# Performance work log

Hardware: AMD Instinct MI355X
Metric: run time of the kernel (lower is better)

The kernel has to match this reference:

```python
import jax, jax.numpy as jnp
import numpy as np

N = 8192   # max_nodes
E = 8192   # max_edges
D = 128    # node / edge feature dim


def setup_inputs() -> dict:
    key = jax.random.key(0)
    ks = jax.random.split(key, 6)
    nodes = jax.random.normal(ks[0], (N, D), jnp.float32)
    edges = jax.random.normal(ks[1], (E, D), jnp.float32)
    send = jax.random.randint(ks[2], (E,), 0, N, jnp.int32)
    rec = jax.random.randint(ks[3], (E,), 0, N, jnp.int32)
    # prefix activity masks (standard for this growing-graph module)
    anodes = (jnp.arange(N) < 6144).astype(jnp.float32)
    aedges = (jnp.arange(E) < 2048).astype(jnp.float32)
    Wq = jax.random.normal(ks[4], (D, D), jnp.float32) / np.sqrt(D)
    bq = jnp.zeros((D,), jnp.float32)
    Wp = jax.random.normal(ks[5], (D, 1), jnp.float32) * 0.1
    bp = jnp.full((1,), -5.0, jnp.float32)
    return dict(nodes=nodes, edges=edges, rec=rec, send=send, anodes=anodes,
                aedges=aedges, Wq=Wq, bq=bq, Wp=Wp, bp=bp)


def reference(nodes, edges, rec, send, anodes, aedges, Wq, bq, Wp, bp):
    # fixed PRNG key (the module takes a key argument; we pin it for determinism)
    key = jax.random.key(42)
    key_prob, key_edges, key_samp = jax.random.split(key, 3)

    nids = jnp.arange(N)
    e_active = aedges.sum().astype(jnp.int32)

    # 1. per-node edge-generation probability: prob_fn(h_i) = sigmoid(h_i @ Wp + bp)
    probs = jax.nn.sigmoid(nodes @ Wp + bp)[:, 0]            # [N]
    # 2. sample generating nodes (only active ones)
    gens = (jax.random.uniform(key_prob, (N,)) < probs * anodes).astype(jnp.float32)

    allowed = E - e_active - 1
    n_gens = jnp.clip(gens.astype(jnp.int32).sum(), 0, allowed)

    # grow active-edge mask by n_gens via repeated (mask @ incr_matrix) clip steps
    # incr_matrix(E) = I + superdiagonal, so one step extends a prefix mask by 1
    mat_e = jnp.eye(E, dtype=jnp.float32) + jnp.eye(E, k=1, dtype=jnp.float32)
    naedges = jax.lax.fori_loop(
        0, n_gens, lambda i, x: jnp.clip(x @ mat_e, 0.0, 1.0), aedges
    ).at[-1].set(0.0)
    mask_new = naedges * (1.0 - aedges)                       # [E] newly-created slots

    # 6. new edges get random embeddings in the newly-activated slots
    new_edges = edges + jax.random.normal(key_edges, edges.shape) * mask_new[:, None]

    # cumsum-derived scatter targets: k-th generating node -> edge slot e_active+k
    gi = gens.astype(jnp.int32)
    trgets = jnp.where(gens > 0, (jnp.cumsum(gens) * gens - gens).astype(jnp.int32), -1) \
             + e_active * gi                                   # [N], -1 dropped by segment_sum

    nsend = jax.ops.segment_sum(nids, trgets, num_segments=E)
    nsend = (send * (1.0 - mask_new) + nsend).astype(jnp.int32)

    # 3-5. queries, all-pairs scores, masked categorical target sampling
    queries = nodes @ Wq + bq                                  # [N, D]
    scores = jnp.clip(queries @ nodes.T, -1e4, 1e4)            # [N, N]
    scores = scores - (1.0 - anodes[None, :]) * 1e10
    select = jnp.where(gens > 0,
                       jax.random.categorical(key_samp, scores, axis=-1),
                       0).astype(jnp.int32)                    # [N]

    nrec = jax.ops.segment_sum(select, trgets, num_segments=E)
    nrec = (rec * (1.0 - mask_new) + nrec).astype(jnp.int32)

    return new_edges, nsend, nrec, naedges
```

## Files before the change

kernel.cpp:

```cpp
#include <hip/hip_runtime.h>
#include <stdint.h>
#include <math.h>

#define NN 8192
#define EE 8192
#define DD 128

__host__ __device__ inline void tf2x32(uint32_t k0, uint32_t k1, uint32_t c0, uint32_t c1,
                                       uint32_t& o0, uint32_t& o1) {
  uint32_t ks[3] = {k0, k1, 0x1BD11BDAu ^ k0 ^ k1};
  uint32_t x0 = c0 + k0, x1 = c1 + k1;
  const uint32_t rot0[4] = {13u, 15u, 26u, 6u};
  const uint32_t rot1[4] = {17u, 29u, 16u, 24u};
#pragma unroll
  for (int i = 0; i < 5; ++i) {
#pragma unroll
    for (int r = 0; r < 4; ++r) {
      uint32_t d = (i & 1) ? rot1[r] : rot0[r];
      x0 += x1;
      x1 = (x1 << d) | (x1 >> (32u - d));
      x1 ^= x0;
    }
    x0 += ks[(i + 1) % 3];
    x1 += ks[(i + 2) % 3] + (uint32_t)(i + 1);
  }
  o0 = x0; o1 = x1;
}

__device__ inline uint32_t rbits32(uint32_t k0, uint32_t k1, uint32_t idx) {
  uint32_t o0, o1;
  tf2x32(k0, k1, 0u, idx, o0, o1);
  return o0 ^ o1;
}

__device__ inline float u01(uint32_t b) {
  return __uint_as_float((b >> 9) | 0x3f800000u) - 1.0f;
}

__device__ inline float erfinv_f32(float x) {
  float w = -log1pf(-x * x);
  float p;
  if (w < 5.0f) {
    w -= 2.5f;
    p = 2.81022636e-08f;
    p = fmaf(p, w, 3.43273939e-07f);
    p = fmaf(p, w, -3.5233877e-06f);
    p = fmaf(p, w, -4.39150654e-06f);
    p = fmaf(p, w, 0.00021858087f);
    p = fmaf(p, w, -0.00125372503f);
    p = fmaf(p, w, -0.00417768164f);
    p = fmaf(p, w, 0.246640727f);
    p = fmaf(p, w, 1.50140941f);
  } else {
    w = sqrtf(w) - 3.0f;
    p = -0.000200214257f;
    p = fmaf(p, w, 0.000100950558f);
    p = fmaf(p, w, 0.00134934322f);
    p = fmaf(p, w, -0.00367342844f);
    p = fmaf(p, w, 0.00573950773f);
    p = fmaf(p, w, -0.0076224613f);
    p = fmaf(p, w, 0.00943887047f);
    p = fmaf(p, w, 1.00167406f);
    p = fmaf(p, w, 2.83297682f);
  }
  return p * x;
}

__global__ __launch_bounds__(256)
void k_gens(const float* __restrict__ nodes, const float* __restrict__ Wp,
            const float* __restrict__ bp, const float* __restrict__ anodes,
            int* __restrict__ gens, uint32_t kp0, uint32_t kp1) {
  int t = blockIdx.x * 256 + threadIdx.x;
  int i = t >> 2, qd = t & 3;
  if (i >= NN) return;
  const float4* row = (const float4*)(nodes + (size_t)i * DD);
  const float4* w = (const float4*)Wp;
  float acc = 0.f;
#pragma unroll
  for (int c = 0; c < 8; ++c) {
    int k4 = qd + 4 * c;
    float4 a = row[k4], b = w[k4];
    acc = fmaf(a.x, b.x, acc); acc = fmaf(a.y, b.y, acc);
    acc = fmaf(a.z, b.z, acc); acc = fmaf(a.w, b.w, acc);
  }
  acc += __shfl_xor(acc, 1, 4);
  acc += __shfl_xor(acc, 2, 4);
  if (qd == 0) {
    float prob = 1.0f / (1.0f + expf(-(acc + bp[0])));
    uint32_t b = rbits32(kp0, kp1, (uint32_t)i);
    gens[i] = (u01(b) < prob * anodes[i]) ? 1 : 0;
  }
}

__global__ __launch_bounds__(256)
void k_scan(const float* __restrict__ aedges, const int* __restrict__ gens,
            int* __restrict__ gen_list, float* __restrict__ mask_new,
            float* __restrict__ naedges_out, int* __restrict__ scal,
            unsigned long long* __restrict__ partial) {
  __shared__ int P[EE];
  __shared__ int aux[8];
  int tid = threadIdx.x;
  int base = tid * 32;
  int lane = tid & 63, wid = tid >> 6;

  int av[32]; int aloc = 0;
  {
    const float4* a4 = (const float4*)(aedges + base);
#pragma unroll
    for (int k4 = 0; k4 < 8; ++k4) {
      float4 x = a4[k4];
      av[4 * k4 + 0] = (x.x > 0.f); av[4 * k4 + 1] = (x.y > 0.f);
      av[4 * k4 + 2] = (x.z > 0.f); av[4 * k4 + 3] = (x.w > 0.f);
    }
#pragma unroll
    for (int k = 0; k < 32; ++k) aloc += av[k];
  }
  int incl = aloc;
#pragma unroll
  for (int d = 1; d < 64; d <<= 1) {
    int o = __shfl_up(incl, d, 64);
    if (lane >= d) incl += o;
  }
  if (lane == 63) aux[wid] = incl;

  int g[32]; int gloc = 0;
  {
    const int4* g4 = (const int4*)(gens + base);
#pragma unroll
    for (int k4 = 0; k4 < 8; ++k4) {
      int4 x = g4[k4];
      g[4 * k4 + 0] = x.x; g[4 * k4 + 1] = x.y;
      g[4 * k4 + 2] = x.z; g[4 * k4 + 3] = x.w;
    }
#pragma unroll
    for (int k = 0; k < 32; ++k) gloc += g[k];
  }
  int incg = gloc;
#pragma unroll
  for (int d = 1; d < 64; d <<= 1) {
    int o = __shfl_up(incg, d, 64);
    if (lane >= d) incg += o;
  }
  if (lane == 63) aux[4 + wid] = incg;
  __syncthreads();

  int e_active = aux[0] + aux[1] + aux[2] + aux[3];
  int total = aux[4] + aux[5] + aux[6] + aux[7];
  int wpreA = 0, wpreG = 0;
  for (int ww = 0; ww < wid; ++ww) { wpreA += aux[ww]; wpreG += aux[4 + ww]; }

  {
    int run = wpreA + incl - aloc;
#pragma unroll
    for (int k = 0; k < 32; ++k) { run += av[k]; P[base + k] = run; }
  }
  {
    int rank = wpreG + incg - gloc;
#pragma unroll
    for (int k = 0; k < 32; ++k) {
      if (g[k]) {
        if (e_active + rank < EE) gen_list[rank] = base + k;
        rank++;
      }
    }
  }
  if (tid == 0) { scal[0] = e_active; scal[1] = total; }

  for (int idx = tid; idx < total * 32; idx += 256) partial[idx] = 0ull;

  int allowed = EE - e_active - 1;
  int n_gens = total;
  if (n_gens > allowed) n_gens = allowed;
  if (n_gens < 0) n_gens = 0;

  __syncthreads();
#pragma unroll
  for (int k = 0; k < 32; ++k) {
    int j = base + k;
    int lo = j - n_gens - 1;
    int wsum = P[j] - (lo >= 0 ? P[lo] : 0);
    float dil = (wsum > 0) ? 1.f : 0.f;
    if (j == EE - 1) dil = 0.f;
    naedges_out[j] = dil;
    mask_new[j] = dil * (1.0f - (float)av[k]);
  }
}

__global__ __launch_bounds__(128)
void k_queries(const float* __restrict__ nodes, const float* __restrict__ Wq,
               const float* __restrict__ bq, const int* __restrict__ gen_list,
               const int* __restrict__ scal, float* __restrict__ queries) {
  __shared__ float ni[DD];
  int tid = threadIdx.x;
  int total = scal[1];
  for (int r = blockIdx.x; r < total; r += gridDim.x) {
    int i = gen_list[r];
    ni[tid] = nodes[(size_t)i * DD + tid];
    __syncthreads();
    float acc = bq[tid];
    for (int k = 0; k < DD; ++k) acc = fmaf(ni[k], Wq[k * DD + tid], acc);
    queries[(size_t)r * DD + tid] = acc;
    __syncthreads();
  }
}

__global__ __launch_bounds__(256)
void k_score(const float* __restrict__ nodes, const float* __restrict__ anodes,
             const float* __restrict__ queries, const int* __restrict__ gen_list,
             const int* __restrict__ scal, unsigned long long* __restrict__ partial,
             uint32_t ks0, uint32_t ks1) {
  __shared__ float4 nd[32 * 32];
  __shared__ float q[8][DD];
  __shared__ float an[32];
  __shared__ int gi[8];
  int tid = threadIdx.x;
  int j0 = blockIdx.x * 32;
  int total = scal[1];
  int rt0 = blockIdx.y * 8;
  if (rt0 >= total) return;

  {
    int jj = tid >> 3, sub = tid & 7;
    const float4* src = (const float4*)(nodes + (size_t)(j0 + jj) * DD);
#pragma unroll
    for (int c = 0; c < 4; ++c) {
      int k4 = sub + 8 * c;
      nd[jj * 32 + ((k4 + jj) & 31)] = src[k4];
    }
    if (tid < 32) an[tid] = anodes[j0 + tid];
  }

  int rr = tid >> 5, jl = tid & 31;
  for (int rb = rt0; rb < total; rb += 8 * gridDim.y) {
    __syncthreads();
    {
      int lr = rb + (tid >> 5);
      int k4 = tid & 31;
      if (lr < total) {
        ((float4*)q[tid >> 5])[k4] = ((const float4*)(queries + (size_t)lr * DD))[k4];
        if (k4 == 0) gi[tid >> 5] = gen_list[lr];
      }
    }
    __syncthreads();

    int r = rb + rr;
    if (r < total) {
      const float4* qv = (const float4*)q[rr];
      float acc = 0.f;
#pragma unroll
      for (int k4 = 0; k4 < 32; ++k4) {
        float4 n = nd[jl * 32 + ((k4 + jl) & 31)];
        float4 qq = qv[k4];
        acc = fmaf(n.x, qq.x, acc); acc = fmaf(n.y, qq.y, acc);
        acc = fmaf(n.z, qq.z, acc); acc = fmaf(n.w, qq.w, acc);
      }
      int j = j0 + jl;
      float sc = fminf(fmaxf(acc, -1e4f), 1e4f);
      sc -= (1.0f - an[jl]) * 1e10f;
      uint32_t bidx = (uint32_t)gi[rr] * NN + (uint32_t)j;
      uint32_t b = rbits32(ks0, ks1, bidx);
      float u = fmaxf(1.17549435e-38f, u01(b));
      float gmb = -logf(-logf(u));
      float v = sc + gmb;
      int jbest = j;
#pragma unroll
      for (int m = 16; m; m >>= 1) {
        float ov = __shfl_xor(v, m, 32);
        int oj = __shfl_xor(jbest, m, 32);
        if (ov > v || (ov == v && oj < jbest)) { v = ov; jbest = oj; }
      }
      if (jl == 0) {
        uint32_t fb = __float_as_uint(v);
        fb = (fb & 0x80000000u) ? ~fb : (fb | 0x80000000u);
        unsigned long long key =
            ((unsigned long long)fb << 32) | (uint32_t)(NN - 1 - jbest);
        atomicMax(&partial[(size_t)r * 32 + (blockIdx.x >> 3)], key);
      }
    }
  }
}

__global__ __launch_bounds__(256)
void k_post(const float* __restrict__ edges, const float* __restrict__ mask_new,
            const int* __restrict__ send, const int* __restrict__ rec,
            const int* __restrict__ gen_list,
            const unsigned long long* __restrict__ partial,
            const int* __restrict__ scal,
            float* __restrict__ out_edges, float* __restrict__ out_nsend,
            float* __restrict__ out_nrec, uint32_t ke0, uint32_t ke1) {
  int t = blockIdx.x * 256 + threadIdx.x;
  int idx = t * 4;
  int e = idx >> 7;
  float m = mask_new[e];
  float4 v = ((const float4*)edges)[t];
  if (m > 0.f) {
    float* pv = &v.x;
#pragma unroll
    for (int k = 0; k < 4; ++k) {
      uint32_t b = rbits32(ke0, ke1, (uint32_t)(idx + k));
      float u = u01(b);
      float x = fmaf(u, 2.0f, -0.99999994f);
      x = fmaxf(-0.99999994f, x);
      float nrm = 1.41421354f * erfinv_f32(x);
      pv[k] += nrm * m;
    }
  }
  ((float4*)out_edges)[t] = v;

  if (t < EE) {
    int e_active = scal[0], total = scal[1];
    float mm = mask_new[t];
    float sf = (float)send[t] * (1.0f - mm);
    float rf = (float)rec[t] * (1.0f - mm);
    int r = t - e_active;
    if (r >= 0 && r < total) {
      unsigned long long best = 0ull;
      const unsigned long long* pp = partial + (size_t)r * 32;
#pragma unroll
      for (int p = 0; p < 32; ++p) { unsigned long long x = pp[p]; if (x > best) best = x; }
      int i = gen_list[r];
      int jsel = (NN - 1) - (int)(best & 0xFFFFFFFFull);
      sf += (float)i;
      rf += (float)jsel;
    }
    out_nsend[t] = (float)(int)sf;
    out_nrec[t] = (float)(int)rf;
  }
}

extern "C" void kernel_launch(void* const* d_in, const int* in_sizes, int n_in,
                              void* d_out, int out_size, void* d_ws, size_t ws_size,
                              hipStream_t stream) {
  const float* nodes  = (const float*)d_in[0];
  const float* edges  = (const float*)d_in[1];
  const int*   rec    = (const int*)d_in[2];
  const int*   send   = (const int*)d_in[3];
  const float* anodes = (const float*)d_in[4];
  const float* aedges = (const float*)d_in[5];
  const float* Wq     = (const float*)d_in[6];
  const float* bq     = (const float*)d_in[7];
  const float* Wp     = (const float*)d_in[8];
  const float* bp     = (const float*)d_in[9];

  float* out        = (float*)d_out;
  float* out_edges  = out;
  float* out_nsend  = out + (size_t)EE * DD;
  float* out_nrec   = out_nsend + EE;
  float* out_naedge = out_nrec + EE;

  char* w = (char*)d_ws;
  int*   gens     = (int*)w;
  int*   gen_list = (int*)(w + 32768);
  int*   scal     = (int*)(w + 65536);
  float* mask_new = (float*)(w + 65792);
  unsigned long long* partial = (unsigned long long*)(w + 98560);
  float* queries  = (float*)(w + 98560 + 6144 * 32 * 8);

  uint32_t kp0, kp1, ke0, ke1, ks0, ks1;
  tf2x32(0u, 42u, 0u, 0u, kp0, kp1);
  tf2x32(0u, 42u, 0u, 1u, ke0, ke1);
  tf2x32(0u, 42u, 0u, 2u, ks0, ks1);

  k_gens<<<NN * 4 / 256, 256, 0, stream>>>(nodes, Wp, bp, anodes, gens, kp0, kp1);
  k_scan<<<1, 256, 0, stream>>>(aedges, gens, gen_list, mask_new, out_naedge, scal, partial);
  k_queries<<<128, 128, 0, stream>>>(nodes, Wq, bq, gen_list, scal, queries);
  k_score<<<dim3(NN / 32, 16), 256, 0, stream>>>(nodes, anodes, queries, gen_list, scal,
                                                 partial, ks0, ks1);
  k_post<<<(EE * DD / 4) / 256, 256, 0, stream>>>(edges, mask_new, send, rec, gen_list,
                                                  partial, scal, out_edges, out_nsend,
                                                  out_nrec, ke0, ke1);
}
```

Before: 43.00 us.

## Fuse query projection into gens kernel and compute queries for all nodes

Merges the per-node probability/sampling kernel with the query projection. Each block now stages 32 node rows in shared memory and computes their full query vectors, so the separate k_queries launch disappears. k_queries had processed one generating node per block in a serial loop. The score kernel now indexes queries by node id through gen_list, and its y-grid is halved. In exchange it computes queries for every node rather than only the few generating ones, and it writes a full N×D queries buffer that must fit in the workspace.

```diff
diff --git a/kernel.cpp b/kernel.cpp
--- a/kernel.cpp
+++ b/kernel.cpp
@@ -67,28 +67,64 @@
 }
 
 __global__ __launch_bounds__(256)
-void k_gens(const float* __restrict__ nodes, const float* __restrict__ Wp,
-            const float* __restrict__ bp, const float* __restrict__ anodes,
-            int* __restrict__ gens, uint32_t kp0, uint32_t kp1) {
-  int t = blockIdx.x * 256 + threadIdx.x;
-  int i = t >> 2, qd = t & 3;
-  if (i >= NN) return;
-  const float4* row = (const float4*)(nodes + (size_t)i * DD);
-  const float4* w = (const float4*)Wp;
-  float acc = 0.f;
-#pragma unroll
-  for (int c = 0; c < 8; ++c) {
-    int k4 = qd + 4 * c;
-    float4 a = row[k4], b = w[k4];
-    acc = fmaf(a.x, b.x, acc); acc = fmaf(a.y, b.y, acc);
-    acc = fmaf(a.z, b.z, acc); acc = fmaf(a.w, b.w, acc);
-  }
-  acc += __shfl_xor(acc, 1, 4);
-  acc += __shfl_xor(acc, 2, 4);
-  if (qd == 0) {
-    float prob = 1.0f / (1.0f + expf(-(acc + bp[0])));
-    uint32_t b = rbits32(kp0, kp1, (uint32_t)i);
-    gens[i] = (u01(b) < prob * anodes[i]) ? 1 : 0;
+void k_gensq(const float* __restrict__ nodes, const float* __restrict__ Wp,
+             const float* __restrict__ bp, const float* __restrict__ anodes,
+             const float* __restrict__ Wq, const float* __restrict__ bq,
+             int* __restrict__ gens, float* __restrict__ queries,
+             uint32_t kp0, uint32_t kp1) {
+  __shared__ float ni[32][DD + 1];
+  int tid = threadIdx.x;
+  int row0 = blockIdx.x * 32;
+
+  {
+    int r = tid >> 3, sub = tid & 7;
+    const float4* src = (const float4*)(nodes + (size_t)(row0 + r) * DD);
+#pragma unroll
+    for (int c = 0; c < 4; ++c) {
+      int k4 = sub + 8 * c;
+      float4 v = src[k4];
+      ni[r][4 * k4 + 0] = v.x; ni[r][4 * k4 + 1] = v.y;
+      ni[r][4 * k4 + 2] = v.z; ni[r][4 * k4 + 3] = v.w;
+    }
+  }
+
+  if (tid < 128) {
+    int i = row0 + (tid >> 2), qd = tid & 3;
+    const float4* row = (const float4*)(nodes + (size_t)i * DD);
+    const float4* w = (const float4*)Wp;
+    float acc = 0.f;
+#pragma unroll
+    for (int c = 0; c < 8; ++c) {
+      int k4 = qd + 4 * c;
+      float4 a = row[k4], b = w[k4];
+      acc = fmaf(a.x, b.x, acc); acc = fmaf(a.y, b.y, acc);
+      acc = fmaf(a.z, b.z, acc); acc = fmaf(a.w, b.w, acc);
+    }
+    acc += __shfl_xor(acc, 1, 4);
+    acc += __shfl_xor(acc, 2, 4);
+    if (qd == 0) {
+      float prob = 1.0f / (1.0f + expf(-(acc + bp[0])));
+      uint32_t b = rbits32(kp0, kp1, (uint32_t)i);
+      gens[i] = (u01(b) < prob * anodes[i]) ? 1 : 0;
+    }
+  }
+  __syncthreads();
+
+  {
+    int col = tid & 127;
+    int rbase = (tid >> 7) * 16;
+    float acc[16];
+    float b0 = bq[col];
+#pragma unroll
+    for (int r = 0; r < 16; ++r) acc[r] = b0;
+    for (int k = 0; k < DD; ++k) {
+      float w = Wq[k * DD + col];
+#pragma unroll
+      for (int r = 0; r < 16; ++r) acc[r] = fmaf(ni[rbase + r][k], w, acc[r]);
+    }
+#pragma unroll
+    for (int r = 0; r < 16; ++r)
+      queries[(size_t)(row0 + rbase + r) * DD + col] = acc[r];
   }
 }
 
@@ -183,24 +219,6 @@
     if (j == EE - 1) dil = 0.f;
     naedges_out[j] = dil;
     mask_new[j] = dil * (1.0f - (float)av[k]);
-  }
-}
-
-__global__ __launch_bounds__(128)
-void k_queries(const float* __restrict__ nodes, const float* __restrict__ Wq,
-               const float* __restrict__ bq, const int* __restrict__ gen_list,
-               const int* __restrict__ scal, float* __restrict__ queries) {
-  __shared__ float ni[DD];
-  int tid = threadIdx.x;
-  int total = scal[1];
-  for (int r = blockIdx.x; r < total; r += gridDim.x) {
-    int i = gen_list[r];
-    ni[tid] = nodes[(size_t)i * DD + tid];
-    __syncthreads();
-    float acc = bq[tid];
-    for (int k = 0; k < DD; ++k) acc = fmaf(ni[k], Wq[k * DD + tid], acc);
-    queries[(size_t)r * DD + tid] = acc;
-    __syncthreads();
   }
 }
 
@@ -237,8 +255,9 @@
       int lr = rb + (tid >> 5);
       int k4 = tid & 31;
       if (lr < total) {
-        ((float4*)q[tid >> 5])[k4] = ((const float4*)(queries + (size_t)lr * DD))[k4];
-        if (k4 == 0) gi[tid >> 5] = gen_list[lr];
+        int id = gen_list[lr];
+        ((float4*)q[tid >> 5])[k4] = ((const float4*)(queries + (size_t)id * DD))[k4];
+        if (k4 == 0) gi[tid >> 5] = id;
       }
     }
     __syncthreads();
@@ -361,11 +380,11 @@
   tf2x32(0u, 42u, 0u, 1u, ke0, ke1);
   tf2x32(0u, 42u, 0u, 2u, ks0, ks1);
 
-  k_gens<<<NN * 4 / 256, 256, 0, stream>>>(nodes, Wp, bp, anodes, gens, kp0, kp1);
+  k_gensq<<<NN / 32, 256, 0, stream>>>(nodes, Wp, bp, anodes, Wq, bq,
+                                       gens, queries, kp0, kp1);
   k_scan<<<1, 256, 0, stream>>>(aedges, gens, gen_list, mask_new, out_naedge, scal, partial);
-  k_queries<<<128, 128, 0, stream>>>(nodes, Wq, bq, gen_list, scal, queries);
-  k_score<<<dim3(NN / 32, 16), 256, 0, stream>>>(nodes, anodes, queries, gen_list, scal,
-                                                 partial, ks0, ks1);
+  k_score<<<dim3(NN / 32, 8), 256, 0, stream>>>(nodes, anodes, queries, gen_list, scal,
+                                                partial, ks0, ks1);
   k_post<<<(EE * DD / 4) / 256, 256, 0, stream>>>(edges, mask_new, send, rec, gen_list,
                                                   partial, scal, out_edges, out_nsend,
                                                   out_nrec, ke0, ke1);
```

Result: slower. 49.48 us (+15.1%).
